# Performance work log

Measured on AMD Instinct MI355X. Metric: run time of the kernel, lower is better.

## Reference

```python
import jax, jax.numpy as jnp
import numpy as np

K = 7          # kernel_size
PAD = 3        # (dilation*(K-1)+1)//2
EPS = 1e-5     # BatchNorm eps
B, CIN, H, W = 4, 256, 56, 56
CR = 32        # rel_planes
COUT = 256     # out_planes
SP = 8         # share_planes
HN = COUT // SP  # attention heads = 32
OFFS = [(dy, dx) for dy in range(K) for dx in range(K)]


def setup_inputs() -> dict:
    key = jax.random.key(0)
    ks = jax.random.split(key, 24)
    def n(i, shape, s=0.05):
        return jax.random.normal(ks[i], shape, dtype=jnp.float32) * s
    def pos(i, shape):  # positive values for BN gamma / running var
        return jax.random.uniform(ks[i], shape, dtype=jnp.float32, minval=0.5, maxval=1.5)
    return {
        "x": jax.random.normal(ks[0], (B, CIN, H, W), dtype=jnp.float32),
        "w1c": n(1, (CR, CIN)),  "b1c": n(2, (CR,)),
        "w2c": n(3, (CR, CIN)),  "b2c": n(4, (CR,)),
        "w3c": n(5, (COUT, CIN)), "b3c": n(6, (COUT,)),
        "bn1_g": pos(7, (CR,)), "bn1_b": n(8, (CR,)), "bn1_m": n(9, (CR,)), "bn1_v": pos(10, (CR,)),
        "cw1": n(11, (CR, CR)),
        "bn2_g": pos(12, (CR,)), "bn2_b": n(13, (CR,)), "bn2_m": n(14, (CR,)), "bn2_v": pos(15, (CR,)),
        "cw2": n(16, (HN, CR)), "cw2_b": n(17, (HN,)),
    }


def _conv1x1(x, w, b):
    # x: [B,C,H,W], w: [O,C]
    return jnp.einsum('bchw,oc->bohw', x, w) + b[None, :, None, None]


def _bn(y, g, b, m, v):
    # inference BatchNorm2d over channel axis 1; y is 4D
    inv = g / jnp.sqrt(v + EPS)
    return y * inv[None, :, None, None] + (b - m * inv)[None, :, None, None]


def reference(x, w1c, b1c, w2c, b2c, w3c, b3c,
              bn1_g, bn1_b, bn1_m, bn1_v, cw1,
              bn2_g, bn2_b, bn2_m, bn2_v, cw2, cw2_b):
    x1 = _conv1x1(x, w1c, b1c)   # [B,CR,H,W]  query
    x2 = _conv1x1(x, w2c, b2c)   # [B,CR,H,W]  key
    x3 = _conv1x1(x, w3c, b3c)   # [B,COUT,H,W] value

    # Subtraction2 with reflection padding (pad_mode=1):
    # diff[b,c,k,i] = x1[b,c,i] - patch_k(x2)[b,c,i]
    x2p = jnp.pad(x2, ((0, 0), (0, 0), (PAD, PAD), (PAD, PAD)), mode='reflect')
    diff = jnp.stack([x1 - x2p[:, :, dy:dy + H, dx:dx + W] for dy, dx in OFFS],
                     axis=2)                      # [B,CR,49,H,W]
    diff = diff.reshape(B, CR, K * K, H * W)      # [B,CR,49,HW]

    # conv_w: BN -> ReLU -> 1x1 conv (no bias) -> BN -> ReLU -> 1x1 conv
    y = jax.nn.relu(_bn(diff, bn1_g, bn1_b, bn1_m, bn1_v))
    y = jnp.einsum('bkln,ok->boln', y, cw1)       # [B,CR,49,HW]
    y = jax.nn.relu(_bn(y, bn2_g, bn2_b, bn2_m, bn2_v))
    logits = jnp.einsum('bkln,ok->boln', y, cw2) + cw2_b[None, :, None, None]
    wgt = jax.nn.softmax(logits, axis=2)          # softmax over k^2, [B,HN,49,HW]
    wgt = wgt.reshape(B, HN, K * K, H, W)

    # Aggregation with reflection padding: out[b,c,i] = sum_k patch_k(x3)[b,c,i] * w[b,c//SP,k,i]
    x3p = jnp.pad(x3, ((0, 0), (0, 0), (PAD, PAD), (PAD, PAD)), mode='reflect')
    out = jnp.zeros((B, HN, SP, H, W), dtype=x.dtype)
    for k, (dy, dx) in enumerate(OFFS):
        patch = x3p[:, :, dy:dy + H, dx:dx + W].reshape(B, HN, SP, H, W)
        out = out + patch * wgt[:, :, k][:, :, None]
    return out.reshape(B, COUT, H, W)
```

## Files before the change

### kernel.cpp

```cpp
#include <hip/hip_runtime.h>
#include <math.h>

#define HW_N   3136
#define W_DIM  56
#define C_IN   256
#define C_R    32
#define C_OUT  256
#define C_ALL  320
#define K2D    49
#define RS     40
#define BN_EPS 1e-5f

typedef _Float16 h2 __attribute__((ext_vector_type(2)));
typedef __fp16  g2 __attribute__((ext_vector_type(2)));
typedef __fp16  g4 __attribute__((ext_vector_type(4)));
typedef __fp16  g8 __attribute__((ext_vector_type(8)));
typedef float   f4 __attribute__((ext_vector_type(4)));

__device__ __forceinline__ h2 pkrtz(float a, float b) {
    g2 r = __builtin_amdgcn_cvt_pkrtz(a, b);
    return __builtin_bit_cast(h2, r);
}

__device__ __forceinline__ g8 pack8(float4 a, float4 b) {
    g2 p0 = __builtin_amdgcn_cvt_pkrtz(a.x, a.y);
    g2 p1 = __builtin_amdgcn_cvt_pkrtz(a.z, a.w);
    g2 p2 = __builtin_amdgcn_cvt_pkrtz(b.x, b.y);
    g2 p3 = __builtin_amdgcn_cvt_pkrtz(b.z, b.w);
    g8 o;
    o[0] = p0[0]; o[1] = p0[1]; o[2] = p1[0]; o[3] = p1[1];
    o[4] = p2[0]; o[5] = p2[1]; o[6] = p3[0]; o[7] = p3[1];
    return o;
}

__device__ __forceinline__ int refl(int v) {
    v = (v < 0) ? -v : v;
    return (v > 55) ? (110 - v) : v;
}

__device__ __forceinline__ void wave_fence() {
    asm volatile("s_waitcnt lgkmcnt(0)" ::: "memory");
}

__global__ __launch_bounds__(256) void k_prep_x(
    const float* __restrict__ x, __fp16* __restrict__ xT16)
{
    const int t   = threadIdx.x;
    const int b   = blockIdx.z;
    const int pos = blockIdx.x * 64 + (t & 63);
    const int ci0 = (blockIdx.y * 4 + (t >> 6)) * 32;
    const float* __restrict__ xp = x + ((size_t)b * C_IN + ci0) * HW_N + pos;
    float v[32];
#pragma unroll
    for (int j = 0; j < 32; ++j) v[j] = xp[(size_t)j * HW_N];
    __fp16* op = xT16 + ((size_t)b * HW_N + pos) * C_IN + ci0;
#pragma unroll
    for (int q = 0; q < 4; ++q) {
        g8 o;
#pragma unroll
        for (int i = 0; i < 4; ++i) {
            const g2 p = __builtin_amdgcn_cvt_pkrtz(v[q * 8 + 2 * i], v[q * 8 + 2 * i + 1]);
            o[2 * i] = p[0]; o[2 * i + 1] = p[1];
        }
        *(g8*)(op + q * 8) = o;
    }
}

__global__ __launch_bounds__(256) void k_conv_mfma(
    const __fp16* __restrict__ xT16,
    const float* __restrict__ w1c, const float* __restrict__ w2c,
    const float* __restrict__ w3c,
    const float* __restrict__ b1c, const float* __restrict__ b2c,
    const float* __restrict__ b3c, __fp16* __restrict__ xall16)
{
    __shared__ __align__(16) float cs[64][68];
    const int t = threadIdx.x, w = t >> 6, lane = t & 63;
    const int quad = lane >> 4, l16 = lane & 15;
    const int b = blockIdx.z, pos0 = blockIdx.x * 64, co0 = blockIdx.y * 64;
    const int co_row = co0 + w * 16 + l16;

    const float* wp = (co_row < 32) ? (w1c + co_row * C_IN)
                    : (co_row < 64) ? (w2c + (co_row - 32) * C_IN)
                                    : (w3c + (co_row - 64) * C_IN);
    const float bias = (co_row < 32) ? b1c[co_row]
                     : (co_row < 64) ? b2c[co_row - 32] : b3c[co_row - 64];

    const __fp16* arow = xT16 + ((size_t)b * HW_N + pos0 + l16) * C_IN + quad * 8;
    const float* brow = wp + quad * 8;

    f4 acc[4];
#pragma unroll
    for (int mt = 0; mt < 4; ++mt) acc[mt] = (f4){0.f, 0.f, 0.f, 0.f};

#pragma unroll
    for (int ks = 0; ks < 8; ++ks) {
        const g8 bf = pack8(*(const float4*)(brow + ks * 32),
                            *(const float4*)(brow + ks * 32 + 4));
#pragma unroll
        for (int mt = 0; mt < 4; ++mt) {
            const g8 af = *(const g8*)(arow + (size_t)mt * 16 * C_IN + ks * 32);
            acc[mt] = __builtin_amdgcn_mfma_f32_16x16x32_f16(af, bf, acc[mt], 0, 0, 0);
        }
    }

#pragma unroll
    for (int mt = 0; mt < 4; ++mt)
#pragma unroll
        for (int r = 0; r < 4; ++r)
            cs[mt * 16 + quad * 4 + r][w * 16 + l16] = acc[mt][r] + bias;
    __syncthreads();

    const int pr = t >> 2, cq = (t & 3) * 16;
    const float4 v0 = *(const float4*)&cs[pr][cq];
    const float4 v1 = *(const float4*)&cs[pr][cq + 4];
    const float4 v2 = *(const float4*)&cs[pr][cq + 8];
    const float4 v3 = *(const float4*)&cs[pr][cq + 12];
    __fp16* op = xall16 + ((size_t)b * HW_N + pos0 + pr) * C_ALL + co0 + cq;
    *(g8*)op = pack8(v0, v1);
    *(g8*)(op + 8) = pack8(v2, v3);
}

__global__ __launch_bounds__(256) void k_attn(
    const __fp16* __restrict__ xq,
    const float* __restrict__ bn1_g, const float* __restrict__ bn1_b,
    const float* __restrict__ bn1_m, const float* __restrict__ bn1_v,
    const float* __restrict__ cw1,
    const float* __restrict__ bn2_g, const float* __restrict__ bn2_b,
    const float* __restrict__ bn2_m, const float* __restrict__ bn2_v,
    const float* __restrict__ cw2, const float* __restrict__ cw2_b,
    float* __restrict__ out)
{
    __shared__ __align__(16) _Float16 tbuf[4][64 * RS];
    __shared__ __align__(16) float stage[4][256];
    __shared__ int pk[4][52];
    const int tid = threadIdx.x;
    const int w = tid >> 6, lane = tid & 63;
    const int b = blockIdx.y;
    const int bid  = blockIdx.x;
    const int posb = (bid & 7) * 98 + (bid >> 3);
    const int pos0 = posb * 4;
    const int pos  = pos0 + w;
    const int y0 = pos / W_DIM, x0 = pos - y0 * W_DIM;
    const __fp16* __restrict__ base16 = xq + (size_t)b * HW_N * C_ALL;
    _Float16* tb = tbuf[w];

    {
        const int c2 = lane & 15;
        const int kh = lane >> 4;
        const float2 g = *(const float2*)(bn1_g + 2 * c2);
        const float2 bb = *(const float2*)(bn1_b + 2 * c2);
        const float2 m = *(const float2*)(bn1_m + 2 * c2);
        const float2 v = *(const float2*)(bn1_v + 2 * c2);
        const float iv0 = g.x * rsqrtf(v.x + BN_EPS), bt0 = bb.x - m.x * iv0;
        const float iv1 = g.y * rsqrtf(v.y + BN_EPS), bt1 = bb.y - m.y * iv1;
        const g2 x1p = *(const g2*)(base16 + (size_t)pos * C_ALL + 2 * c2);
        const float x1a = (float)x1p[0], x1b = (float)x1p[1];
#pragma unroll
        for (int j = 0; j < 13; ++j) {
            const int k = 4 * j + kh;
            if (k < K2D) {
                const int dy = k / 7, dx = k - dy * 7;
                const int rp = refl(y0 + dy - 3) * W_DIM + refl(x0 + dx - 3);
                if (c2 == 0) pk[w][k] = rp;
                const g2 x2p = *(const g2*)(base16 + (size_t)rp * C_ALL + 32 + 2 * c2);
                const float t0 = fmaxf((x1a - (float)x2p[0]) * iv0 + bt0, 0.f);
                const float t1 = fmaxf((x1b - (float)x2p[1]) * iv1 + bt1, 0.f);
                *(h2*)&tb[k * RS + 2 * c2] = pkrtz(t0, t1);
            }
        }
    }
    wave_fence();

    const int quad = lane >> 4, l16 = lane & 15;
    f4 acc[4][2];

    {
        g8 bf[2];
#pragma unroll
        for (int nt = 0; nt < 2; ++nt) {
            const float* wr = cw1 + (nt * 16 + l16) * C_R + quad * 8;
            bf[nt] = pack8(*(const float4*)wr, *(const float4*)(wr + 4));
        }
#pragma unroll
        for (int mt = 0; mt < 4; ++mt) {
            acc[mt][0] = (f4){0.f, 0.f, 0.f, 0.f};
            acc[mt][1] = (f4){0.f, 0.f, 0.f, 0.f};
            const g8 af = *(const g8*)((const __fp16*)tb + (mt * 16 + l16) * RS + quad * 8);
            acc[mt][0] = __builtin_amdgcn_mfma_f32_16x16x32_f16(af, bf[0], acc[mt][0], 0, 0, 0);
            acc[mt][1] = __builtin_amdgcn_mfma_f32_16x16x32_f16(af, bf[1], acc[mt][1], 0, 0, 0);
        }
    }
    wave_fence();

#pragma unroll
    for (int nt = 0; nt < 2; ++nt) {
        const int o = nt * 16 + l16;
        const float iv = bn2_g[o] * rsqrtf(bn2_v[o] + BN_EPS);
        const float bt = bn2_b[o] - bn2_m[o] * iv;
#pragma unroll
        for (int mt = 0; mt < 4; ++mt)
#pragma unroll
            for (int r = 0; r < 4; ++r) {
                const int row = mt * 16 + quad * 4 + r;
                tb[row * RS + o] = (_Float16)fmaxf(acc[mt][nt][r] * iv + bt, 0.f);
            }
    }
    wave_fence();

    {
        g8 bf[2];
#pragma unroll
        for (int nt = 0; nt < 2; ++nt) {
            const float* wr = cw2 + (nt * 16 + l16) * C_R + quad * 8;
            bf[nt] = pack8(*(const float4*)wr, *(const float4*)(wr + 4));
        }
#pragma unroll
        for (int mt = 0; mt < 4; ++mt) {
            acc[mt][0] = (f4){0.f, 0.f, 0.f, 0.f};
            acc[mt][1] = (f4){0.f, 0.f, 0.f, 0.f};
            const g8 af = *(const g8*)((const __fp16*)tb + (mt * 16 + l16) * RS + quad * 8);
            acc[mt][0] = __builtin_amdgcn_mfma_f32_16x16x32_f16(af, bf[0], acc[mt][0], 0, 0, 0);
            acc[mt][1] = __builtin_amdgcn_mfma_f32_16x16x32_f16(af, bf[1], acc[mt][1], 0, 0, 0);
        }
    }
    wave_fence();

#pragma unroll
    for (int nt = 0; nt < 2; ++nt) {
        const float bsv = cw2_b[nt * 16 + l16];
        float m = -1e30f;
#pragma unroll
        for (int mt = 0; mt < 4; ++mt)
#pragma unroll
            for (int r = 0; r < 4; ++r) {
                const int k = mt * 16 + quad * 4 + r;
                const float v = acc[mt][nt][r] + bsv;
                acc[mt][nt][r] = v;
                if (k < K2D) m = fmaxf(m, v);
            }
        m = fmaxf(m, __shfl_xor(m, 16, 64));
        m = fmaxf(m, __shfl_xor(m, 32, 64));
        float s = 0.f;
#pragma unroll
        for (int mt = 0; mt < 4; ++mt)
#pragma unroll
            for (int r = 0; r < 4; ++r) {
                const int k = mt * 16 + quad * 4 + r;
                const float e = (k < K2D) ? __expf(acc[mt][nt][r] - m) : 0.f;
                acc[mt][nt][r] = e;
                s += e;
            }
        s += __shfl_xor(s, 16, 64);
        s += __shfl_xor(s, 32, 64);
        const float rs = 1.f / s;
        const int o = nt * 16 + l16;
#pragma unroll
        for (int mt = 0; mt < 4; ++mt)
#pragma unroll
            for (int r = 0; r < 4; ++r) {
                const int row = mt * 16 + quad * 4 + r;
                tb[row * RS + o] = (_Float16)(acc[mt][nt][r] * rs);
            }
    }
    wave_fence();

    {
        const int hn = lane >> 1;
        float4 a = make_float4(0.f, 0.f, 0.f, 0.f);
#pragma unroll 7
        for (int k = 0; k < K2D; ++k) {
            const int rp = pk[w][k];
            const float wv = (float)tb[k * RS + hn];
            const g4 v = *(const g4*)(base16 + (size_t)rp * C_ALL + 64 + lane * 4);
            a.x += (float)v[0] * wv; a.y += (float)v[1] * wv;
            a.z += (float)v[2] * wv; a.w += (float)v[3] * wv;
        }
        *(float4*)&stage[w][lane * 4] = a;
    }
    __syncthreads();

    {
        const int c = tid;
        float4 o;
        o.x = stage[0][c]; o.y = stage[1][c];
        o.z = stage[2][c]; o.w = stage[3][c];
        *(float4*)(out + ((size_t)b * C_OUT + c) * HW_N + pos0) = o;
    }
}

extern "C" void kernel_launch(void* const* d_in, const int* in_sizes, int n_in,
                              void* d_out, int out_size, void* d_ws, size_t ws_size,
                              hipStream_t stream)
{
    const float* x     = (const float*)d_in[0];
    const float* w1c   = (const float*)d_in[1];
    const float* b1c   = (const float*)d_in[2];
    const float* w2c   = (const float*)d_in[3];
    const float* b2c   = (const float*)d_in[4];
    const float* w3c   = (const float*)d_in[5];
    const float* b3c   = (const float*)d_in[6];
    const float* bn1_g = (const float*)d_in[7];
    const float* bn1_b = (const float*)d_in[8];
    const float* bn1_m = (const float*)d_in[9];
    const float* bn1_v = (const float*)d_in[10];
    const float* cw1   = (const float*)d_in[11];
    const float* bn2_g = (const float*)d_in[12];
    const float* bn2_b = (const float*)d_in[13];
    const float* bn2_m = (const float*)d_in[14];
    const float* bn2_v = (const float*)d_in[15];
    const float* cw2   = (const float*)d_in[16];
    const float* cw2_b = (const float*)d_in[17];

    __fp16* xT16   = (__fp16*)d_ws;
    __fp16* xall16 = xT16 + (size_t)4 * HW_N * C_IN;

    k_prep_x<<<dim3(49, 2, 4), 256, 0, stream>>>(x, xT16);
    k_conv_mfma<<<dim3(49, 5, 4), 256, 0, stream>>>(xT16, w1c, w2c, w3c,
                                                    b1c, b2c, b3c, xall16);
    k_attn<<<dim3(784, 4, 1), 256, 0, stream>>>(xall16,
        bn1_g, bn1_b, bn1_m, bn1_v, cw1,
        bn2_g, bn2_b, bn2_m, bn2_v, cw2, cw2_b, (float*)d_out);
}
```

Before: 167.7 us.

## Use packed fp16 math and transposed weight buffer in attention kernel

The BN1+ReLU stage now runs as packed half-precision FMAs, each lane handling 8 channels with 16-byte loads instead of 2 channels with 4-byte loads. The softmax weights are stored transposed (head-major, stride 72) so the aggregation loop can read 8 weights per vector load. Aggregation accumulates in packed fp16 over groups of 8 taps and then folds into fp32. This cuts conversions, instruction count and LDS traffic, at the cost of fp16 rounding in the BN and in the partial sums.

```diff
diff --git a/kernel.cpp b/kernel.cpp
--- a/kernel.cpp
+++ b/kernel.cpp
@@ -9,9 +9,12 @@
 #define C_ALL  320
 #define K2D    49
 #define RS     40
+#define WTS    72
 #define BN_EPS 1e-5f
 
 typedef _Float16 h2 __attribute__((ext_vector_type(2)));
+typedef _Float16 h4 __attribute__((ext_vector_type(4)));
+typedef _Float16 h8 __attribute__((ext_vector_type(8)));
 typedef __fp16  g2 __attribute__((ext_vector_type(2)));
 typedef __fp16  g4 __attribute__((ext_vector_type(4)));
 typedef __fp16  g8 __attribute__((ext_vector_type(8)));
@@ -145,27 +148,47 @@
     _Float16* tb = tbuf[w];
 
     {
-        const int c2 = lane & 15;
-        const int kh = lane >> 4;
-        const float2 g = *(const float2*)(bn1_g + 2 * c2);
-        const float2 bb = *(const float2*)(bn1_b + 2 * c2);
-        const float2 m = *(const float2*)(bn1_m + 2 * c2);
-        const float2 v = *(const float2*)(bn1_v + 2 * c2);
-        const float iv0 = g.x * rsqrtf(v.x + BN_EPS), bt0 = bb.x - m.x * iv0;
-        const float iv1 = g.y * rsqrtf(v.y + BN_EPS), bt1 = bb.y - m.y * iv1;
-        const g2 x1p = *(const g2*)(base16 + (size_t)pos * C_ALL + 2 * c2);
-        const float x1a = (float)x1p[0], x1b = (float)x1p[1];
-#pragma unroll
-        for (int j = 0; j < 13; ++j) {
-            const int k = 4 * j + kh;
+        const int r16 = lane >> 2;
+        const int q8  = (lane & 3) * 8;
+        float G[8], Bb[8], M[8], V[8], ivt[8], prt[8];
+        *(float4*)&G[0]  = *(const float4*)(bn1_g + q8);
+        *(float4*)&G[4]  = *(const float4*)(bn1_g + q8 + 4);
+        *(float4*)&Bb[0] = *(const float4*)(bn1_b + q8);
+        *(float4*)&Bb[4] = *(const float4*)(bn1_b + q8 + 4);
+        *(float4*)&M[0]  = *(const float4*)(bn1_m + q8);
+        *(float4*)&M[4]  = *(const float4*)(bn1_m + q8 + 4);
+        *(float4*)&V[0]  = *(const float4*)(bn1_v + q8);
+        *(float4*)&V[4]  = *(const float4*)(bn1_v + q8 + 4);
+        const g8 x1v = *(const g8*)(base16 + (size_t)pos * C_ALL + q8);
+#pragma unroll
+        for (int i = 0; i < 8; ++i) {
+            ivt[i] = G[i] * rsqrtf(V[i] + BN_EPS);
+            prt[i] = (float)x1v[i] * ivt[i] + (Bb[i] - M[i] * ivt[i]);
+        }
+        h2 niv[4], pre[4];
+#pragma unroll
+        for (int j = 0; j < 4; ++j) {
+            niv[j] = pkrtz(-ivt[2 * j], -ivt[2 * j + 1]);
+            pre[j] = pkrtz(prt[2 * j], prt[2 * j + 1]);
+        }
+        const h2 z = (h2)(_Float16)0;
+#pragma unroll
+        for (int p = 0; p < 4; ++p) {
+            const int k = p * 16 + r16;
             if (k < K2D) {
                 const int dy = k / 7, dx = k - dy * 7;
                 const int rp = refl(y0 + dy - 3) * W_DIM + refl(x0 + dx - 3);
-                if (c2 == 0) pk[w][k] = rp;
-                const g2 x2p = *(const g2*)(base16 + (size_t)rp * C_ALL + 32 + 2 * c2);
-                const float t0 = fmaxf((x1a - (float)x2p[0]) * iv0 + bt0, 0.f);
-                const float t1 = fmaxf((x1b - (float)x2p[1]) * iv1 + bt1, 0.f);
-                *(h2*)&tb[k * RS + 2 * c2] = pkrtz(t0, t1);
+                if (q8 == 0) pk[w][k] = rp;
+                union { g8 v; g2 p2[4]; } u;
+                u.v = *(const g8*)(base16 + (size_t)rp * C_ALL + 32 + q8);
+                h8 tt;
+#pragma unroll
+                for (int j = 0; j < 4; ++j) {
+                    h2 tj = __builtin_bit_cast(h2, u.p2[j]) * niv[j] + pre[j];
+                    tj = __builtin_elementwise_max(tj, z);
+                    tt[2 * j] = tj[0]; tt[2 * j + 1] = tj[1];
+                }
+                *(h8*)(tb + k * RS + q8) = tt;
             }
         }
     }
@@ -253,29 +276,40 @@
         s += __shfl_xor(s, 16, 64);
         s += __shfl_xor(s, 32, 64);
         const float rs = 1.f / s;
-        const int o = nt * 16 + l16;
-#pragma unroll
-        for (int mt = 0; mt < 4; ++mt)
-#pragma unroll
-            for (int r = 0; r < 4; ++r) {
-                const int row = mt * 16 + quad * 4 + r;
-                tb[row * RS + o] = (_Float16)(acc[mt][nt][r] * rs);
-            }
+        const int h = nt * 16 + l16;
+#pragma unroll
+        for (int mt = 0; mt < 4; ++mt) {
+            const h2 w01 = pkrtz(acc[mt][nt][0] * rs, acc[mt][nt][1] * rs);
+            const h2 w23 = pkrtz(acc[mt][nt][2] * rs, acc[mt][nt][3] * rs);
+            h4 ww; ww[0] = w01[0]; ww[1] = w01[1]; ww[2] = w23[0]; ww[3] = w23[1];
+            *(h4*)(tb + h * WTS + mt * 16 + quad * 4) = ww;
+        }
     }
     wave_fence();
 
     {
         const int hn = lane >> 1;
-        float4 a = make_float4(0.f, 0.f, 0.f, 0.f);
-#pragma unroll 7
-        for (int k = 0; k < K2D; ++k) {
-            const int rp = pk[w][k];
-            const float wv = (float)tb[k * RS + hn];
-            const g4 v = *(const g4*)(base16 + (size_t)rp * C_ALL + 64 + lane * 4);
-            a.x += (float)v[0] * wv; a.y += (float)v[1] * wv;
-            a.z += (float)v[2] * wv; a.w += (float)v[3] * wv;
-        }
-        *(float4*)&stage[w][lane * 4] = a;
+        const _Float16* wrow = tb + hn * WTS;
+        const __fp16* x3p = base16 + 64 + lane * 4;
+        float fx = 0.f, fy = 0.f, fz = 0.f, fw = 0.f;
+#pragma unroll
+        for (int kb = 0; kb < 7; ++kb) {
+            const h8 wv = *(const h8*)(wrow + kb * 8);
+            h2 a01 = (h2)(_Float16)0, a23 = (h2)(_Float16)0;
+            const int jmax = (kb == 6) ? 1 : 8;
+#pragma unroll
+            for (int j = 0; j < jmax; ++j) {
+                const int rp = pk[w][kb * 8 + j];
+                union { g4 v; g2 p[2]; } u;
+                u.v = *(const g4*)(x3p + (size_t)rp * C_ALL);
+                const h2 wp = (h2){wv[j], wv[j]};
+                a01 = __builtin_bit_cast(h2, u.p[0]) * wp + a01;
+                a23 = __builtin_bit_cast(h2, u.p[1]) * wp + a23;
+            }
+            fx += (float)a01[0]; fy += (float)a01[1];
+            fz += (float)a23[0]; fw += (float)a23[1];
+        }
+        *(float4*)&stage[w][lane * 4] = make_float4(fx, fy, fz, fw);
     }
     __syncthreads();
 
```

After: 169.5 us. About the same (+1.1%).

## Fuse fp16 transpose of x into the 1x1 conv MFMA kernel

Applied to the files above, without the earlier changes.

Removes the separate prep kernel that transposed x to a position-major fp16 buffer. The conv kernel now loads fp32 x directly, converts it to fp16 and stores it in XOR-swizzled shared memory. Each block covers 32 positions and all 320 output channels, with each wave computing 80 channels. This avoids one launch and the global round trip of the transposed buffer, and reads x only once per position tile. In exchange there are fewer blocks (392), more weight loads per block, and higher register pressure from 10 accumulators.

```diff
diff --git a/kernel.cpp b/kernel.cpp
--- a/kernel.cpp
+++ b/kernel.cpp
@@ -42,82 +42,96 @@
     asm volatile("s_waitcnt lgkmcnt(0)" ::: "memory");
 }
 
-__global__ __launch_bounds__(256) void k_prep_x(
-    const float* __restrict__ x, __fp16* __restrict__ xT16)
-{
-    const int t   = threadIdx.x;
-    const int b   = blockIdx.z;
-    const int pos = blockIdx.x * 64 + (t & 63);
-    const int ci0 = (blockIdx.y * 4 + (t >> 6)) * 32;
-    const float* __restrict__ xp = x + ((size_t)b * C_IN + ci0) * HW_N + pos;
-    float v[32];
-#pragma unroll
-    for (int j = 0; j < 32; ++j) v[j] = xp[(size_t)j * HW_N];
-    __fp16* op = xT16 + ((size_t)b * HW_N + pos) * C_IN + ci0;
-#pragma unroll
-    for (int q = 0; q < 4; ++q) {
-        g8 o;
-#pragma unroll
-        for (int i = 0; i < 4; ++i) {
-            const g2 p = __builtin_amdgcn_cvt_pkrtz(v[q * 8 + 2 * i], v[q * 8 + 2 * i + 1]);
-            o[2 * i] = p[0]; o[2 * i + 1] = p[1];
-        }
-        *(g8*)(op + q * 8) = o;
-    }
-}
-
 __global__ __launch_bounds__(256) void k_conv_mfma(
-    const __fp16* __restrict__ xT16,
+    const float* __restrict__ x,
     const float* __restrict__ w1c, const float* __restrict__ w2c,
     const float* __restrict__ w3c,
     const float* __restrict__ b1c, const float* __restrict__ b2c,
     const float* __restrict__ b3c, __fp16* __restrict__ xall16)
 {
-    __shared__ __align__(16) float cs[64][68];
+    __shared__ __align__(16) _Float16 smem[32 * 328];
     const int t = threadIdx.x, w = t >> 6, lane = t & 63;
     const int quad = lane >> 4, l16 = lane & 15;
-    const int b = blockIdx.z, pos0 = blockIdx.x * 64, co0 = blockIdx.y * 64;
-    const int co_row = co0 + w * 16 + l16;
-
-    const float* wp = (co_row < 32) ? (w1c + co_row * C_IN)
-                    : (co_row < 64) ? (w2c + (co_row - 32) * C_IN)
-                                    : (w3c + (co_row - 64) * C_IN);
-    const float bias = (co_row < 32) ? b1c[co_row]
-                     : (co_row < 64) ? b2c[co_row - 32] : b3c[co_row - 64];
-
-    const __fp16* arow = xT16 + ((size_t)b * HW_N + pos0 + l16) * C_IN + quad * 8;
-    const float* brow = wp + quad * 8;
-
-    f4 acc[4];
-#pragma unroll
-    for (int mt = 0; mt < 4; ++mt) acc[mt] = (f4){0.f, 0.f, 0.f, 0.f};
-
+    const int b = blockIdx.z, pos0 = blockIdx.x * 32;
+
+    {
+        const int p = t & 31;
+        const int gb = t >> 5;
+        const float* xp = x + (size_t)b * C_IN * HW_N + pos0 + p;
+#pragma unroll
+        for (int i = 0; i < 4; ++i) {
+            const int g = i * 8 + gb;
+            const int ci = g * 8;
+            float v[8];
+#pragma unroll
+            for (int j = 0; j < 8; ++j) v[j] = xp[(size_t)(ci + j) * HW_N];
+            g8 o;
+#pragma unroll
+            for (int jj = 0; jj < 4; ++jj) {
+                const g2 pr = __builtin_amdgcn_cvt_pkrtz(v[2 * jj], v[2 * jj + 1]);
+                o[2 * jj] = pr[0]; o[2 * jj + 1] = pr[1];
+            }
+            *(g8*)((__fp16*)smem + (size_t)(p * 32 + (g ^ (p & 7))) * 8) = o;
+        }
+    }
+    __syncthreads();
+
+    const float* wrow[5]; float bias[5];
+#pragma unroll
+    for (int nt = 0; nt < 5; ++nt) {
+        const int co = w * 80 + nt * 16 + l16;
+        wrow[nt] = (co < 32) ? (w1c + co * C_IN)
+                 : (co < 64) ? (w2c + (co - 32) * C_IN)
+                             : (w3c + (co - 64) * C_IN);
+        bias[nt] = (co < 32) ? b1c[co] : (co < 64) ? b2c[co - 32] : b3c[co - 64];
+    }
+
+    f4 acc[2][5];
+#pragma unroll
+    for (int mt = 0; mt < 2; ++mt)
+#pragma unroll
+        for (int nt = 0; nt < 5; ++nt) acc[mt][nt] = (f4){0.f, 0.f, 0.f, 0.f};
+
+    const int xo = l16 & 7;
 #pragma unroll
     for (int ks = 0; ks < 8; ++ks) {
-        const g8 bf = pack8(*(const float4*)(brow + ks * 32),
-                            *(const float4*)(brow + ks * 32 + 4));
-#pragma unroll
-        for (int mt = 0; mt < 4; ++mt) {
-            const g8 af = *(const g8*)(arow + (size_t)mt * 16 * C_IN + ks * 32);
-            acc[mt] = __builtin_amdgcn_mfma_f32_16x16x32_f16(af, bf, acc[mt], 0, 0, 0);
-        }
-    }
-
-#pragma unroll
-    for (int mt = 0; mt < 4; ++mt)
-#pragma unroll
-        for (int r = 0; r < 4; ++r)
-            cs[mt * 16 + quad * 4 + r][w * 16 + l16] = acc[mt][r] + bias;
+        g8 bf[5];
+#pragma unroll
+        for (int nt = 0; nt < 5; ++nt) {
+            const float* wp = wrow[nt] + ks * 32 + quad * 8;
+            bf[nt] = pack8(*(const float4*)wp, *(const float4*)(wp + 4));
+        }
+#pragma unroll
+        for (int mt = 0; mt < 2; ++mt) {
+            const int row = mt * 16 + l16;
+            const g8 af = *(const g8*)((const __fp16*)smem
+                          + (size_t)(row * 32 + ((ks * 4 + quad) ^ xo)) * 8);
+#pragma unroll
+            for (int nt = 0; nt < 5; ++nt)
+                acc[mt][nt] = __builtin_amdgcn_mfma_f32_16x16x32_f16(af, bf[nt], acc[mt][nt], 0, 0, 0);
+        }
+    }
     __syncthreads();
 
-    const int pr = t >> 2, cq = (t & 3) * 16;
-    const float4 v0 = *(const float4*)&cs[pr][cq];
-    const float4 v1 = *(const float4*)&cs[pr][cq + 4];
-    const float4 v2 = *(const float4*)&cs[pr][cq + 8];
-    const float4 v3 = *(const float4*)&cs[pr][cq + 12];
-    __fp16* op = xall16 + ((size_t)b * HW_N + pos0 + pr) * C_ALL + co0 + cq;
-    *(g8*)op = pack8(v0, v1);
-    *(g8*)(op + 8) = pack8(v2, v3);
+#pragma unroll
+    for (int mt = 0; mt < 2; ++mt)
+#pragma unroll
+        for (int nt = 0; nt < 5; ++nt) {
+            const int co = w * 80 + nt * 16 + l16;
+#pragma unroll
+            for (int r = 0; r < 4; ++r) {
+                const int row = mt * 16 + quad * 4 + r;
+                smem[row * 328 + co] = (_Float16)(acc[mt][nt][r] + bias[nt]);
+            }
+        }
+    __syncthreads();
+#pragma unroll
+    for (int i = 0; i < 5; ++i) {
+        const int idx = i * 256 + t;
+        const int row = idx / 40, c8 = idx - row * 40;
+        const g8 v = *(const g8*)((const __fp16*)smem + row * 328 + c8 * 8);
+        *(g8*)(xall16 + ((size_t)b * HW_N + pos0 + row) * C_ALL + c8 * 8) = v;
+    }
 }
 
 __global__ __launch_bounds__(256) void k_attn(
@@ -311,11 +325,9 @@
     const float* cw2   = (const float*)d_in[16];
     const float* cw2_b = (const float*)d_in[17];
 
-    __fp16* xT16   = (__fp16*)d_ws;
-    __fp16* xall16 = xT16 + (size_t)4 * HW_N * C_IN;
-
-    k_prep_x<<<dim3(49, 2, 4), 256, 0, stream>>>(x, xT16);
-    k_conv_mfma<<<dim3(49, 5, 4), 256, 0, stream>>>(xT16, w1c, w2c, w3c,
+    __fp16* xall16 = (__fp16*)d_ws;
+
+    k_conv_mfma<<<dim3(98, 1, 4), 256, 0, stream>>>(x, w1c, w2c, w3c,
                                                     b1c, b2c, b3c, xall16);
     k_attn<<<dim3(784, 4, 1), 256, 0, stream>>>(xall16,
         bn1_g, bn1_b, bn1_m, bn1_v, cw1,
```

Result: faster. 159.2 us (-5.0%).
